# Performance work log

Measured on AMD Instinct MI355X. Metric: run time of the kernel, lower is better.

The kernel has to match this reference:

```python
import jax, jax.numpy as jnp
import numpy as np
import math

# ---- model constants (match init_kwargs) ----
B, T, HID = 2, 4096, 2048
H, D = 16, 128            # heads, head_dim; num_kv_heads == H
ROPE_DIM = 64             # head_dim * partial_rotary_factor (0.5)
THETA = 10000.0
EPS = 1e-6
CHUNK = 64                # chunk size for the chunked simple-GLA scan
LAYER_IDX, N_LAYERS = 12, 32


def _alibi_slopes(n):
    # power-of-2 path of build_slope_tensor
    start = 2.0 ** (-(2.0 ** -(math.log2(n) - 3.0)))
    return np.array([start ** (i + 1) for i in range(n)], dtype=np.float32)


def _layer_slope():
    scale = 1.0 - (LAYER_IDX - 1) / (N_LAYERS - 1) + 1e-5
    return jnp.asarray(-_alibi_slopes(H) * scale)  # [H], negative log-decay per step


def _rmsnorm(x, w):
    xf = x.astype(jnp.float32)
    var = jnp.mean(xf * xf, axis=-1, keepdims=True)
    return (w * (xf * jax.lax.rsqrt(var + EPS)).astype(x.dtype))


def _group_rmsnorm(x, w, groups):
    # x: [..., groups*gd]; normalize within each group, then elementwise weight
    shp = x.shape
    xg = x.reshape(shp[:-1] + (groups, shp[-1] // groups)).astype(jnp.float32)
    var = jnp.mean(xg * xg, axis=-1, keepdims=True)
    xn = (xg * jax.lax.rsqrt(var + EPS)).astype(x.dtype).reshape(shp)
    return w * xn


def _rope_cos_sin(position_ids):
    inv_freq = 1.0 / (THETA ** (jnp.arange(0, ROPE_DIM, 2, dtype=jnp.float32) / ROPE_DIM))
    freqs = position_ids.astype(jnp.float32)[..., None] * inv_freq  # [B,T,ROPE_DIM/2]
    emb = jnp.concatenate([freqs, freqs], axis=-1)                  # [B,T,ROPE_DIM]
    return jnp.cos(emb), jnp.sin(emb)


def _rotate_half(x):
    x1, x2 = jnp.split(x, 2, axis=-1)
    return jnp.concatenate([-x2, x1], axis=-1)


def _apply_rope(x, cos, sin):
    # x: [B,T,H,D]; partial rotary on first ROPE_DIM dims
    c = cos[:, :, None, :]
    s = sin[:, :, None, :]
    x_rot, x_pass = x[..., :ROPE_DIM], x[..., ROPE_DIM:]
    x_rot = x_rot * c + _rotate_half(x_rot) * s
    return jnp.concatenate([x_rot, x_pass], axis=-1)


def _chunk_simple_gla(q, k, v, slope):
    # q,k,v: [B,T,H,D]; slope: [H] (negative per-step log-decay)
    # recurrence: S_t = exp(slope)*S_{t-1} + k_t^T v_t ; o_t = q_t S_t
    q = q * (D ** -0.5)
    nc = T // CHUNK
    def to_chunks(x):
        # [B,T,H,D] -> [nc,B,H,CHUNK,D]
        return x.reshape(B, nc, CHUNK, H, D).transpose(1, 0, 3, 2, 4)
    qc, kc, vc = to_chunks(q), to_chunks(k), to_chunks(v)

    i = jnp.arange(CHUNK, dtype=jnp.float32)
    g = slope[:, None, None]                                  # [H,1,1]
    mask = jnp.where(i[:, None] >= i[None, :],
                     jnp.exp(g * (i[:, None] - i[None, :])), 0.0)   # [H,C,C]
    q_dec = jnp.exp(slope[:, None] * (i + 1.0))               # [H,C]
    k_dec = jnp.exp(slope[:, None] * (CHUNK - 1.0 - i))       # [H,C]
    ch_dec = jnp.exp(slope * CHUNK)                           # [H]

    S0 = jnp.zeros((B, H, D, D), q.dtype)

    def step(S, inp):
        qi, ki, vi = inp                                       # [B,H,C,D]
        att = jnp.einsum('bhcd,bhed->bhce', qi, ki) * mask[None]
        intra = jnp.einsum('bhce,bhed->bhcd', att, vi)
        inter = jnp.einsum('bhcd,bhde->bhce', qi * q_dec[None, :, :, None], S)
        S_new = ch_dec[None, :, None, None] * S + \
            jnp.einsum('bhcd,bhce->bhde', ki * k_dec[None, :, :, None], vi)
        return S_new, intra + inter

    _, o = jax.lax.scan(step, S0, (qc, kc, vc))                # o: [nc,B,H,C,D]
    return o.transpose(1, 0, 3, 2, 4).reshape(B, T, H * D)


def setup_inputs() -> dict:
    key = jax.random.key(0)
    ks = jax.random.split(key, 4)
    return {
        'hidden_states': jax.random.normal(ks[0], (B, T, HID), jnp.float32),
        'w_qkv': jax.random.normal(ks[1], (3 * H * D, HID), jnp.float32) * 0.02,
        'q_ln_w': jnp.ones((D,), jnp.float32),
        'k_ln_w': jnp.ones((D,), jnp.float32),
        'g_norm_w': jnp.ones((H * D,), jnp.float32),
        'w_g_proj': jax.random.normal(ks[2], (H * D, HID), jnp.float32) * 0.02,
        'w_dense': jax.random.normal(ks[3], (HID, H * D), jnp.float32) * 0.02,
        'position_ids': jnp.arange(B * T, dtype=jnp.int32).reshape(B, T) % T,
    }


def reference(hidden_states, w_qkv, q_ln_w, k_ln_w, g_norm_w, w_g_proj, w_dense, position_ids):
    slope = _layer_slope()
    qkv = jnp.einsum('bth,oh->bto', hidden_states, w_qkv)
    q, k, v = jnp.split(qkv, [H * D, 2 * H * D], axis=-1)
    q = q.reshape(B, T, H, D)
    k = k.reshape(B, T, H, D)
    v = v.reshape(B, T, H, D)
    # qk-norm (per-head RMSNorm)
    q = _rmsnorm(q, q_ln_w)
    k = _rmsnorm(k, k_ln_w)
    # partial RoPE
    cos, sin = _rope_cos_sin(position_ids)
    q = _apply_rope(q, cos, sin)
    k = _apply_rope(k, cos, sin)
    # chunked lightning (simple-GLA) linear attention
    o = _chunk_simple_gla(q, k, v, slope)                      # [B,T,H*D]
    # group RMSNorm (per head) + sigmoid output gate, then output proj
    gate = jax.nn.sigmoid(jnp.einsum('bth,oh->bto', hidden_states, w_g_proj))
    o = _group_rmsnorm(o, g_norm_w, groups=H) * gate
    return jnp.einsum('bto,ho->bth', o, w_dense)
```

## Files before the change

### kernel.cpp

```cpp
#include <hip/hip_runtime.h>
#include <math.h>

typedef short bf16x8 __attribute__((ext_vector_type(8)));
typedef float f32x4 __attribute__((ext_vector_type(4)));

#define LOG2E 1.4426950408889634f
#define GSCALE 0.6451712903225806f

__device__ __forceinline__ float bf2f(unsigned short h) {
    union { unsigned u; float f; } v; v.u = ((unsigned)h) << 16; return v.f;
}
__device__ __forceinline__ unsigned short f2bf(float f) {
    union { float f; unsigned u; } v; v.f = f;
    unsigned r = v.u + 0x7FFFu + ((v.u >> 16) & 1u);
    return (unsigned short)(r >> 16);
}

#define GLD16(lds, g)                                                          \
    __builtin_amdgcn_global_load_lds(                                          \
        (const __attribute__((address_space(1))) void*)(g),                    \
        (__attribute__((address_space(3))) void*)(lds), 16, 0, 0)

#define MFMA16(a, b, c) __builtin_amdgcn_mfma_f32_16x16x32_bf16(a, b, c, 0, 0, 0)

struct us4 { unsigned short a, b, c, d; };
__global__ __launch_bounds__(256) void cvt4_f32_bf16(
    const float* __restrict__ s0, const float* __restrict__ s1,
    const float* __restrict__ s2, const float* __restrict__ s3,
    unsigned short* __restrict__ dst, int c0, int c1, int c2, int n4)
{
    int i = blockIdx.x * 256 + threadIdx.x;
    if (i >= n4) return;
    const float* s; int off;
    if (i < c0)      { s = s0; off = i; }
    else if (i < c1) { s = s1; off = i - c0; }
    else if (i < c2) { s = s2; off = i - c1; }
    else             { s = s3; off = i - c2; }
    float4 v = ((const float4*)s)[off];
    us4 o = { f2bf(v.x), f2bf(v.y), f2bf(v.z), f2bf(v.w) };
    ((us4*)dst)[i] = o;
}

template <int EPI>
__global__ __launch_bounds__(256) void gemm_bt(
    const unsigned short* __restrict__ A, const unsigned short* __restrict__ Bt,
    void* __restrict__ Cv,
    unsigned short* __restrict__ Qp, unsigned short* __restrict__ Kp,
    unsigned short* __restrict__ Vp, unsigned short* __restrict__ Gb,
    int M, int N, int K)
{
    __shared__ __attribute__((aligned(16))) unsigned short lA[128 * 64];
    __shared__ __attribute__((aligned(16))) unsigned short lB[128 * 64];
    const int tid  = threadIdx.x;
    const int bn   = blockIdx.x, bm = blockIdx.y;
    const int lane = tid & 63, wave = tid >> 6;
    const int quad = lane >> 4, lr = lane & 15;
    const int wm   = (wave >> 1) * 64, wn = (wave & 1) * 64;
    const int lsw  = lr & 7;
    f32x4 acc[4][4] = {};

    const unsigned short* Abase = A + ((long long)bm * 128) * K;
    const unsigned short* Bbase = Bt + ((long long)bn * 128) * K;

    for (int kt = 0; kt < K; kt += 64) {
        __syncthreads();
#pragma unroll
        for (int r = 0; r < 4; ++r) {
            int c   = r * 256 + tid;
            int row = c >> 3, g = c & 7;
            int gg  = (g ^ (row & 7)) * 8;
            GLD16(lA + c * 8, Abase + (long long)row * K + kt + gg);
            GLD16(lB + c * 8, Bbase + (long long)row * K + kt + gg);
        }
        __syncthreads();
#pragma unroll
        for (int s = 0; s < 2; ++s) {
            bf16x8 af[4], bfv[4];
#pragma unroll
            for (int i = 0; i < 4; ++i)
                af[i] = *(const bf16x8*)(lA + (wm + i * 16 + lr) * 64 +
                                         (((s * 4 + quad) ^ lsw) * 8));
#pragma unroll
            for (int j = 0; j < 4; ++j)
                bfv[j] = *(const bf16x8*)(lB + (wn + j * 16 + lr) * 64 +
                                          (((s * 4 + quad) ^ lsw) * 8));
#pragma unroll
            for (int i = 0; i < 4; ++i)
#pragma unroll
                for (int j = 0; j < 4; ++j)
                    acc[i][j] = MFMA16(af[i], bfv[j], acc[i][j]);
        }
    }

#pragma unroll
    for (int i = 0; i < 4; ++i)
#pragma unroll
        for (int j = 0; j < 4; ++j)
#pragma unroll
            for (int r = 0; r < 4; ++r) {
                int row = bm * 128 + wm + i * 16 + quad * 4 + r;
                int col = bn * 128 + wn + j * 16 + lr;
                float v = acc[i][j][r];
                if (EPI == 0) {
                    if (col < 6144) {
                        int tens = col >> 11, h = (col >> 7) & 15, e = col & 127;
                        int b = row >> 12, t = row & 4095;
                        long long dst = (((long long)(b * 16 + h)) * 4096 + t) * 128 + e;
                        unsigned short* P = (tens == 0) ? Qp : ((tens == 1) ? Kp : Vp);
                        P[dst] = f2bf(v);
                    } else {
                        v = 1.0f / (1.0f + __expf(-v));
                        Gb[(long long)row * 2048 + (col - 6144)] = f2bf(v);
                    }
                } else {
                    ((float*)Cv)[(long long)row * N + col] = v;
                }
            }
}

__global__ __launch_bounds__(256) void norm_rope(
    unsigned short* __restrict__ Qp, unsigned short* __restrict__ Kp,
    const float* __restrict__ qw, const float* __restrict__ kw,
    const int* __restrict__ pos_ids)
{
    const int bid  = blockIdx.x;
    const int tg   = bid & 1023, h = (bid >> 10) & 15, b = bid >> 14;
    const int wave = threadIdx.x >> 6, lane = threadIdx.x & 63;
    const int t    = tg * 4 + wave;
    const long long rowbase = (((long long)(b * 16 + h)) * 4096 + t) * 128;
    const int pos = pos_ids[b * 4096 + t];
    const int d0  = lane * 2;

    float c0 = 1.f, s0 = 0.f, c1 = 1.f, s1 = 0.f;
    if (lane < 32) {
        float fj0 = (float)(d0 & 31), fj1 = (float)((d0 + 1) & 31);
        float if0 = exp2f(-fj0 * 0.4152410118609203f);
        float if1 = exp2f(-fj1 * 0.4152410118609203f);
        sincosf((float)pos * if0, &s0, &c0);
        sincosf((float)pos * if1, &s1, &c1);
    }
    const float w0q = qw[d0], w1q = qw[d0 + 1];
    const float w0k = kw[d0], w1k = kw[d0 + 1];

#pragma unroll
    for (int which = 0; which < 2; ++which) {
        unsigned short* P = which ? Kp : Qp;
        float w0 = which ? w0k : w0q, w1 = which ? w1k : w1q;
        unsigned u = *(const unsigned*)(P + rowbase + d0);
        float x0 = bf2f(u & 0xFFFF), x1 = bf2f(u >> 16);
        float ss = x0 * x0 + x1 * x1;
#pragma unroll
        for (int off = 32; off; off >>= 1) ss += __shfl_xor(ss, off);
        float r  = rsqrtf(ss * (1.0f / 128.0f) + 1e-6f);
        float xn0 = x0 * r * w0;
        float xn1 = x1 * r * w1;
        float p0 = __shfl_xor(xn0, 16);
        float p1 = __shfl_xor(xn1, 16);
        float y0, y1;
        if (d0 < 32)      { y0 = xn0 * c0 - p0 * s0; y1 = xn1 * c1 - p1 * s1; }
        else if (d0 < 64) { y0 = xn0 * c0 + p0 * s0; y1 = xn1 * c1 + p1 * s1; }
        else              { y0 = xn0; y1 = xn1; }
        if (which == 0) { y0 *= 0.08838834764831845f; y1 *= 0.08838834764831845f; }
        *(unsigned*)(P + rowbase + d0) =
            (unsigned)f2bf(y0) | ((unsigned)f2bf(y1) << 16);
    }
}

__global__ __launch_bounds__(256) void gla_chunk(
    const unsigned short* __restrict__ Qp, const unsigned short* __restrict__ Kp,
    const unsigned short* __restrict__ Vp,
    unsigned short* __restrict__ Oint, unsigned short* __restrict__ Ubuf)
{
    __shared__ __attribute__((aligned(16))) unsigned short sK[64 * 136];
    __shared__ __attribute__((aligned(16))) unsigned short sVT[128 * 72];
    __shared__ __attribute__((aligned(16))) unsigned short sKT[128 * 72];
    __shared__ __attribute__((aligned(16))) unsigned short sAtt[64 * 72];

    const int bid = blockIdx.x;
    const int n = bid & 63, h = (bid >> 6) & 15, b = bid >> 10;
    const int tid = threadIdx.x, wave = tid >> 6, lane = tid & 63;
    const int quad = lane >> 4, lr = lane & 15;
    const float gl2 = -exp2f(-0.5f * (float)(h + 1)) * GSCALE * LOG2E;

    const long long rb = (((long long)(b * 16 + h)) * 4096 + (long long)n * 64) * 128;

    const int cS = wave * 16 + lr;
    const float qsc = exp2f(gl2 * (float)cS);
    bf16x8 qf[4];
#pragma unroll
    for (int ks = 0; ks < 4; ++ks) {
        union { uint4 v; unsigned short s[8]; } in, ou;
        in.v = *(const uint4*)(Qp + rb + cS * 128 + ks * 32 + quad * 8);
#pragma unroll
        for (int j = 0; j < 8; ++j) ou.s[j] = f2bf(bf2f(in.s[j]) * qsc);
        qf[ks] = *(bf16x8*)&ou;
    }
#pragma unroll
    for (int rr = 0; rr < 4; ++rr) {
        int idx = rr * 256 + tid;
        int c = idx >> 4, d8 = (idx & 15) << 3;
        *(uint4*)(sK + c * 136 + d8) = *(const uint4*)(Kp + rb + c * 128 + d8);
    }
#pragma unroll
    for (int rr = 0; rr < 4; ++rr) {
        int idx = rr * 256 + tid;
        int c = idx & 63, g8 = (idx >> 6) << 3;
        union { uint4 v; unsigned short s[8]; } vv, kk;
        vv.v = *(const uint4*)(Vp + rb + c * 128 + g8);
        kk.v = *(const uint4*)(Kp + rb + c * 128 + g8);
        float kdsc = exp2f(gl2 * (float)(64 - c));
#pragma unroll
        for (int j = 0; j < 8; ++j) {
            sVT[(g8 + j) * 72 + c] = vv.s[j];
            sKT[(g8 + j) * 72 + c] = f2bf(bf2f(kk.s[j]) * kdsc);
        }
    }
    __syncthreads();

    f32x4 aacc[4] = {};
#pragma unroll
    for (int nj = 0; nj < 4; ++nj)
#pragma unroll
        for (int ks = 0; ks < 4; ++ks) {
            bf16x8 bf = *(const bf16x8*)(sK + (nj * 16 + lr) * 136 + ks * 32 + quad * 8);
            aacc[nj] = MFMA16(qf[ks], bf, aacc[nj]);
        }
#pragma unroll
    for (int nj = 0; nj < 4; ++nj) {
        int c2 = nj * 16 + lr;
        float colf = exp2f(-gl2 * (float)c2);
#pragma unroll
        for (int r = 0; r < 4; ++r) {
            int c = wave * 16 + quad * 4 + r;
            sAtt[c * 72 + c2] = f2bf((c >= c2) ? aacc[nj][r] * colf : 0.0f);
        }
    }
    f32x4 Sacc[2][8] = {};
#pragma unroll
    for (int me = 0; me < 2; ++me)
#pragma unroll
        for (int ks = 0; ks < 2; ++ks) {
            bf16x8 af = *(const bf16x8*)(sVT + (wave * 32 + me * 16 + lr) * 72 + ks * 32 + quad * 8);
#pragma unroll
            for (int dj = 0; dj < 8; ++dj) {
                bf16x8 bf = *(const bf16x8*)(sKT + (dj * 16 + lr) * 72 + ks * 32 + quad * 8);
                Sacc[me][dj] = MFMA16(af, bf, Sacc[me][dj]);
            }
        }
    const long long ub = ((long long)((b * 16 + h) * 64 + n)) * 16384;
#pragma unroll
    for (int me = 0; me < 2; ++me)
#pragma unroll
        for (int r = 0; r < 4; ++r) {
            int e = wave * 32 + me * 16 + quad * 4 + r;
#pragma unroll
            for (int dj = 0; dj < 8; ++dj)
                Ubuf[ub + e * 128 + dj * 16 + lr] = f2bf(Sacc[me][dj][r]);
        }
    __syncthreads();

    f32x4 oacc[8] = {};
#pragma unroll
    for (int ks = 0; ks < 2; ++ks) {
        bf16x8 af = *(const bf16x8*)(sAtt + cS * 72 + ks * 32 + quad * 8);
#pragma unroll
        for (int ej = 0; ej < 8; ++ej) {
            bf16x8 bf = *(const bf16x8*)(sVT + (ej * 16 + lr) * 72 + ks * 32 + quad * 8);
            oacc[ej] = MFMA16(af, bf, oacc[ej]);
        }
    }
#pragma unroll
    for (int ej = 0; ej < 8; ++ej)
#pragma unroll
        for (int r = 0; r < 4; ++r) {
            int c = wave * 16 + quad * 4 + r;
            long long off = ((long long)(b * 4096 + n * 64 + c)) * 2048 + h * 128 + ej * 16 + lr;
            Oint[off] = f2bf(oacc[ej][r]);
        }
}

__global__ __launch_bounds__(256) void gla_scan(
    const unsigned short* __restrict__ Ubuf, unsigned short* __restrict__ STbuf)
{
    const int bid = blockIdx.x;
    const int es = bid & 7, bh = bid >> 3;
    const int h = bh & 15;
    const float gl2 = -exp2f(-0.5f * (float)(h + 1)) * GSCALE * LOG2E;
    const float chd = exp2f(gl2 * 64.0f);
    const int tid = threadIdx.x;
    const long long base = (long long)bh * 64 * 16384 + es * 2048 + tid * 8;
    float st[8] = {};
    for (int n = 0; n < 64; ++n) {
        long long a = base + (long long)n * 16384;
        union { uint4 v; unsigned short s[8]; } u, o;
        u.v = *(const uint4*)(Ubuf + a);
#pragma unroll
        for (int j = 0; j < 8; ++j) o.s[j] = f2bf(st[j]);
        *(uint4*)(STbuf + a) = o.v;
#pragma unroll
        for (int j = 0; j < 8; ++j) st[j] = st[j] * chd + bf2f(u.s[j]);
    }
}

__global__ __launch_bounds__(256) void gla_inter(
    const unsigned short* __restrict__ Qp, const unsigned short* __restrict__ STbuf,
    unsigned short* __restrict__ Ob, const unsigned short* __restrict__ Gb,
    const float* __restrict__ W)
{
    __shared__ __attribute__((aligned(16))) unsigned short sST[128 * 136];
    const int bid = blockIdx.x;
    const int n = bid & 63, h = (bid >> 6) & 15, b = bid >> 10;
    const int tid = threadIdx.x, wave = tid >> 6, lane = tid & 63;
    const int quad = lane >> 4, lr = lane & 15;
    const float gl2 = -exp2f(-0.5f * (float)(h + 1)) * GSCALE * LOG2E;
    const long long rb = (((long long)(b * 16 + h)) * 4096 + (long long)n * 64) * 128;
    const long long stb = ((long long)((b * 16 + h) * 64 + n)) * 16384;

#pragma unroll
    for (int rr = 0; rr < 8; ++rr) {
        int idx = rr * 256 + tid;
        int row = idx >> 4, d8 = (idx & 15) << 3;
        *(uint4*)(sST + row * 136 + d8) = *(const uint4*)(STbuf + stb + row * 128 + d8);
    }
    const int cS = wave * 16 + lr;
    const float qsc = exp2f(gl2 * (float)cS);
    bf16x8 qf[4];
#pragma unroll
    for (int ks = 0; ks < 4; ++ks) {
        union { uint4 v; unsigned short s[8]; } in, ou;
        in.v = *(const uint4*)(Qp + rb + cS * 128 + ks * 32 + quad * 8);
#pragma unroll
        for (int j = 0; j < 8; ++j) ou.s[j] = f2bf(bf2f(in.s[j]) * qsc);
        qf[ks] = *(bf16x8*)&ou;
    }
    __syncthreads();

    f32x4 oacc[8] = {};
#pragma unroll
    for (int ks = 0; ks < 4; ++ks)
#pragma unroll
        for (int ej = 0; ej < 8; ++ej) {
            bf16x8 bf = *(const bf16x8*)(sST + (ej * 16 + lr) * 136 + ks * 32 + quad * 8);
            oacc[ej] = MFMA16(qf[ks], bf, oacc[ej]);
        }

    float w[8];
#pragma unroll
    for (int ej = 0; ej < 8; ++ej) w[ej] = W[h * 128 + ej * 16 + lr];

    float ss[4] = {};
#pragma unroll
    for (int r = 0; r < 4; ++r) {
        int c = wave * 16 + quad * 4 + r;
        long long off = ((long long)(b * 4096 + n * 64 + c)) * 2048 + h * 128;
#pragma unroll
        for (int ej = 0; ej < 8; ++ej) {
            float v = oacc[ej][r] + bf2f(Ob[off + ej * 16 + lr]);
            oacc[ej][r] = v;
            ss[r] += v * v;
        }
    }
#pragma unroll
    for (int r = 0; r < 4; ++r) {
#pragma unroll
        for (int o2 = 1; o2 < 16; o2 <<= 1) ss[r] += __shfl_xor(ss[r], o2);
        float rn = rsqrtf(ss[r] * (1.0f / 128.0f) + 1e-6f);
        int c = wave * 16 + quad * 4 + r;
        long long off = ((long long)(b * 4096 + n * 64 + c)) * 2048 + h * 128;
#pragma unroll
        for (int ej = 0; ej < 8; ++ej) {
            float g = bf2f(Gb[off + ej * 16 + lr]);
            Ob[off + ej * 16 + lr] = f2bf(oacc[ej][r] * rn * w[ej] * g);
        }
    }
}

extern "C" void kernel_launch(void* const* d_in, const int* in_sizes, int n_in,
                              void* d_out, int out_size, void* d_ws, size_t ws_size,
                              hipStream_t stream)
{
    const float* hid   = (const float*)d_in[0];
    const float* w_qkv = (const float*)d_in[1];
    const float* q_ln  = (const float*)d_in[2];
    const float* k_ln  = (const float*)d_in[3];
    const float* g_nw  = (const float*)d_in[4];
    const float* w_g   = (const float*)d_in[5];
    const float* w_d   = (const float*)d_in[6];
    const int*   pos   = (const int*)d_in[7];

    const size_t PLANE = (size_t)2 * 16 * 4096 * 128;
    unsigned short* Qp    = (unsigned short*)d_ws;
    unsigned short* Kp    = Qp + PLANE;
    unsigned short* Vp    = Kp + PLANE;
    unsigned short* Ob    = Vp + PLANE;
    unsigned short* Gb    = Ob + PLANE;
    unsigned short* hidb  = Gb + PLANE;
    unsigned short* wqkvb = hidb + (size_t)8192 * 2048;
    unsigned short* wgb   = wqkvb + (size_t)6144 * 2048;
    unsigned short* wdb   = wgb + (size_t)2048 * 2048;
    unsigned short* Ubuf  = hidb;
    unsigned short* STbuf = Kp;

    dim3 blk(256);
    const int c0 = 8192 * 2048 / 4;
    const int c1 = c0 + 6144 * 2048 / 4;
    const int c2 = c1 + 2048 * 2048 / 4;
    const int n4 = c2 + 2048 * 2048 / 4;
    cvt4_f32_bf16<<<(n4 + 255) / 256, blk, 0, stream>>>(
        hid, w_qkv, w_g, w_d, hidb, c0, c1, c2, n4);

    gemm_bt<0><<<dim3(64, 64), blk, 0, stream>>>(hidb, wqkvb, nullptr, Qp, Kp, Vp,
                                                 Gb, 8192, 8192, 2048);
    norm_rope<<<32768, blk, 0, stream>>>(Qp, Kp, q_ln, k_ln, pos);
    gla_chunk<<<2048, blk, 0, stream>>>(Qp, Kp, Vp, Ob, Ubuf);
    gla_scan<<<256, blk, 0, stream>>>(Ubuf, STbuf);
    gla_inter<<<2048, blk, 0, stream>>>(Qp, STbuf, Ob, Gb, g_nw);
    gemm_bt<2><<<dim3(16, 64), blk, 0, stream>>>(Ob, wdb, d_out, nullptr, nullptr,
                                                 nullptr, nullptr, 8192, 2048, 2048);
}
```

Before: 701.6 us.

## Replace GEMM with 256x256 double-buffered pipelined kernel and XCD tile swizzle

Replaces the 128x128 single-buffered GEMM with a 256x256 tile, 512-thread kernel that double-buffers LDS and interleaves async global-to-LDS loads with MFMA quarters, using manual barriers, waitcnt and setprio scheduling. Block indices are swizzled across XCDs to improve L2 locality. This aims to hide memory latency and raise arithmetic intensity in both projections. The cost is heavier register and LDS use (128KB LDS per block) and fragile hand-tuned waitcnt ordering. The output GEMM launches only 256 blocks, which may underfill the device.

```diff
diff --git a/kernel.cpp b/kernel.cpp
--- a/kernel.cpp
+++ b/kernel.cpp
@@ -42,80 +42,141 @@
 }
 
 template <int EPI>
-__global__ __launch_bounds__(256) void gemm_bt(
+__global__ __launch_bounds__(512, 2) void gemm256(
     const unsigned short* __restrict__ A, const unsigned short* __restrict__ Bt,
     void* __restrict__ Cv,
     unsigned short* __restrict__ Qp, unsigned short* __restrict__ Kp,
     unsigned short* __restrict__ Vp, unsigned short* __restrict__ Gb,
     int M, int N, int K)
 {
-    __shared__ __attribute__((aligned(16))) unsigned short lA[128 * 64];
-    __shared__ __attribute__((aligned(16))) unsigned short lB[128 * 64];
+    __shared__ __attribute__((aligned(16))) unsigned short lA[2][16384];
+    __shared__ __attribute__((aligned(16))) unsigned short lB[2][16384];
+
     const int tid  = threadIdx.x;
-    const int bn   = blockIdx.x, bm = blockIdx.y;
     const int lane = tid & 63, wave = tid >> 6;
     const int quad = lane >> 4, lr = lane & 15;
-    const int wm   = (wave >> 1) * 64, wn = (wave & 1) * 64;
+    const int wm   = (wave >> 2) * 128;
+    const int wn   = (wave & 3) * 64;
     const int lsw  = lr & 7;
-    f32x4 acc[4][4] = {};
-
-    const unsigned short* Abase = A + ((long long)bm * 128) * K;
-    const unsigned short* Bbase = Bt + ((long long)bn * 128) * K;
-
-    for (int kt = 0; kt < K; kt += 64) {
-        __syncthreads();
-#pragma unroll
-        for (int r = 0; r < 4; ++r) {
-            int c   = r * 256 + tid;
-            int row = c >> 3, g = c & 7;
-            int gg  = (g ^ (row & 7)) * 8;
-            GLD16(lA + c * 8, Abase + (long long)row * K + kt + gg);
-            GLD16(lB + c * 8, Bbase + (long long)row * K + kt + gg);
-        }
-        __syncthreads();
-#pragma unroll
-        for (int s = 0; s < 2; ++s) {
-            bf16x8 af[4], bfv[4];
-#pragma unroll
-            for (int i = 0; i < 4; ++i)
-                af[i] = *(const bf16x8*)(lA + (wm + i * 16 + lr) * 64 +
-                                         (((s * 4 + quad) ^ lsw) * 8));
-#pragma unroll
-            for (int j = 0; j < 4; ++j)
-                bfv[j] = *(const bf16x8*)(lB + (wn + j * 16 + lr) * 64 +
-                                          (((s * 4 + quad) ^ lsw) * 8));
-#pragma unroll
-            for (int i = 0; i < 4; ++i)
-#pragma unroll
-                for (int j = 0; j < 4; ++j)
-                    acc[i][j] = MFMA16(af[i], bfv[j], acc[i][j]);
-        }
-    }
-
-#pragma unroll
-    for (int i = 0; i < 4; ++i)
+
+    const int nwg = (int)(gridDim.x * gridDim.y);
+    const int lin = (int)(blockIdx.y * gridDim.x + blockIdx.x);
+    const int swz = (lin & 7) * (nwg >> 3) + (lin >> 3);
+    const int bn = swz % (int)gridDim.x, bm = swz / (int)gridDim.x;
+
+    const unsigned short* Ab = A  + (long long)bm * 256 * K;
+    const unsigned short* Bb = Bt + (long long)bn * 256 * K;
+
+    const int c0r = tid, c1r = 512 + tid;
+    const int row0 = c0r >> 3, row1 = c1r >> 3;
+    const long long ga0 = (long long)row0 * K + ((c0r & 7) ^ (row0 & 7)) * 8;
+    const long long ga1 = (long long)row1 * K + ((c1r & 7) ^ (row1 & 7)) * 8;
+    const long long HK  = (long long)128 * K;
+    const int l0 = c0r * 8, l1 = c1r * 8;
+
+#define STAGE(ldsb, gb, half, kt)                                              \
+    do {                                                                       \
+        GLD16((ldsb) + (half) * 8192 + l0, (gb) + (half) * HK + (kt) + ga0);   \
+        GLD16((ldsb) + (half) * 8192 + l1, (gb) + (half) * HK + (kt) + ga1);   \
+    } while (0)
+
+    f32x4 acc[8][4] = {};
+    bf16x8 a[4][2], blo[2][2], bhi[2][2];
+
+#define LOADA(buf, base)                                                       \
+    _Pragma("unroll") for (int i = 0; i < 4; ++i)                              \
+    _Pragma("unroll") for (int s = 0; s < 2; ++s)                              \
+        a[i][s] = *(const bf16x8*)((buf) + ((base) + i * 16 + lr) * 64 +       \
+                                   (((s * 4 + quad) ^ lsw) * 8));
+#define LOADB(dst, buf, base)                                                  \
+    _Pragma("unroll") for (int j = 0; j < 2; ++j)                              \
+    _Pragma("unroll") for (int s = 0; s < 2; ++s)                              \
+        dst[j][s] = *(const bf16x8*)((buf) + ((base) + j * 16 + lr) * 64 +     \
+                                     (((s * 4 + quad) ^ lsw) * 8));
+#define MFMAQ(MQ, NQ, BV)                                                      \
+    _Pragma("unroll") for (int i = 0; i < 4; ++i)                              \
+    _Pragma("unroll") for (int j = 0; j < 2; ++j)                              \
+    _Pragma("unroll") for (int s = 0; s < 2; ++s)                              \
+        acc[(MQ) * 4 + i][(NQ) * 2 + j] =                                      \
+            MFMA16(a[i][s], BV[j][s], acc[(MQ) * 4 + i][(NQ) * 2 + j]);
+
+#define BARR()  asm volatile("s_barrier" ::: "memory")
+#define LGKM0() asm volatile("s_waitcnt lgkmcnt(0)" ::: "memory")
+#define VM6()   asm volatile("s_waitcnt vmcnt(6)" ::: "memory")
+#define PTAIL() do { BARR(); LGKM0(); __builtin_amdgcn_sched_barrier(0);       \
+                     __builtin_amdgcn_s_setprio(1); } while (0)
+#define PEND()  do { __builtin_amdgcn_s_setprio(0); BARR(); } while (0)
+
+    STAGE(lA[0], Ab, 0, 0); STAGE(lA[0], Ab, 1, 0);
+    STAGE(lB[0], Bb, 0, 0); STAGE(lB[0], Bb, 1, 0);
+    STAGE(lB[1], Bb, 0, 64); STAGE(lB[1], Bb, 1, 64);
+    STAGE(lA[1], Ab, 0, 64);
+    VM6();
+    BARR();
+
+    const int NT = K >> 6;
+    for (int it = 0; it < (NT >> 1); ++it) {
+        const int v   = 2 * it + 1;
+        const int kn0 = (2 * it + 2 < NT) ? (2 * it + 2) * 64 : 0;
+        const int kn1 = (2 * it + 3 < NT) ? (2 * it + 3) * 64 : 0;
+        LOADA(lA[0], wm); LOADB(blo, lB[0], wn);
+        STAGE(lA[1], Ab, 1, v * 64);
+        PTAIL(); MFMAQ(0, 0, blo); PEND();
+        LOADB(bhi, lB[0], wn + 32);
+        PTAIL(); MFMAQ(0, 1, bhi); PEND();
+        LOADA(lA[0], wm + 64);
+        STAGE(lB[0], Bb, 0, kn0);
+        PTAIL(); MFMAQ(1, 1, bhi); PEND();
+        STAGE(lB[0], Bb, 1, kn0); STAGE(lA[0], Ab, 0, kn0);
+        VM6(); BARR();
+        __builtin_amdgcn_s_setprio(1); MFMAQ(1, 0, blo); PEND();
+        LOADA(lA[1], wm); LOADB(blo, lB[1], wn);
+        STAGE(lA[0], Ab, 1, kn0);
+        PTAIL(); MFMAQ(0, 0, blo); PEND();
+        LOADB(bhi, lB[1], wn + 32);
+        PTAIL(); MFMAQ(0, 1, bhi); PEND();
+        LOADA(lA[1], wm + 64);
+        STAGE(lB[1], Bb, 0, kn1);
+        PTAIL(); MFMAQ(1, 1, bhi); PEND();
+        STAGE(lB[1], Bb, 1, kn1); STAGE(lA[1], Ab, 0, kn1);
+        VM6(); BARR();
+        __builtin_amdgcn_s_setprio(1); MFMAQ(1, 0, blo); PEND();
+    }
+    asm volatile("s_waitcnt vmcnt(0)" ::: "memory");
+
+#pragma unroll
+    for (int i = 0; i < 8; ++i)
 #pragma unroll
         for (int j = 0; j < 4; ++j)
 #pragma unroll
             for (int r = 0; r < 4; ++r) {
-                int row = bm * 128 + wm + i * 16 + quad * 4 + r;
-                int col = bn * 128 + wn + j * 16 + lr;
-                float v = acc[i][j][r];
+                int row = bm * 256 + wm + i * 16 + quad * 4 + r;
+                int col = bn * 256 + wn + j * 16 + lr;
+                float vv = acc[i][j][r];
                 if (EPI == 0) {
                     if (col < 6144) {
                         int tens = col >> 11, h = (col >> 7) & 15, e = col & 127;
                         int b = row >> 12, t = row & 4095;
                         long long dst = (((long long)(b * 16 + h)) * 4096 + t) * 128 + e;
                         unsigned short* P = (tens == 0) ? Qp : ((tens == 1) ? Kp : Vp);
-                        P[dst] = f2bf(v);
+                        P[dst] = f2bf(vv);
                     } else {
-                        v = 1.0f / (1.0f + __expf(-v));
-                        Gb[(long long)row * 2048 + (col - 6144)] = f2bf(v);
+                        vv = 1.0f / (1.0f + __expf(-vv));
+                        Gb[(long long)row * 2048 + (col - 6144)] = f2bf(vv);
                     }
                 } else {
-                    ((float*)Cv)[(long long)row * N + col] = v;
+                    ((float*)Cv)[(long long)row * N + col] = vv;
                 }
             }
+#undef STAGE
+#undef LOADA
+#undef LOADB
+#undef MFMAQ
+#undef BARR
+#undef LGKM0
+#undef VM6
+#undef PTAIL
+#undef PEND
 }
 
 __global__ __launch_bounds__(256) void norm_rope(
@@ -409,12 +470,12 @@
     cvt4_f32_bf16<<<(n4 + 255) / 256, blk, 0, stream>>>(
         hid, w_qkv, w_g, w_d, hidb, c0, c1, c2, n4);
 
-    gemm_bt<0><<<dim3(64, 64), blk, 0, stream>>>(hidb, wqkvb, nullptr, Qp, Kp, Vp,
-                                                 Gb, 8192, 8192, 2048);
+    gemm256<0><<<dim3(32, 32), dim3(512), 0, stream>>>(
+        hidb, wqkvb, nullptr, Qp, Kp, Vp, Gb, 8192, 8192, 2048);
     norm_rope<<<32768, blk, 0, stream>>>(Qp, Kp, q_ln, k_ln, pos);
     gla_chunk<<<2048, blk, 0, stream>>>(Qp, Kp, Vp, Ob, Ubuf);
     gla_scan<<<256, blk, 0, stream>>>(Ubuf, STbuf);
     gla_inter<<<2048, blk, 0, stream>>>(Qp, STbuf, Ob, Gb, g_nw);
-    gemm_bt<2><<<dim3(16, 64), blk, 0, stream>>>(Ob, wdb, d_out, nullptr, nullptr,
-                                                 nullptr, nullptr, 8192, 2048, 2048);
-}
+    gemm256<2><<<dim3(8, 32), dim3(512), 0, stream>>>(
+        Ob, wdb, d_out, nullptr, nullptr, nullptr, nullptr, 8192, 2048, 2048);
+}
```

New measurement: 656.0 us. 1.07x faster.
